# Kernel optimization log

Hardware: AMD Instinct MI355X
Metric: run time of the kernel (lower is better)

The kernel has to match this reference:

```python
import jax, jax.numpy as jnp
import numpy as np
import math

H, DK, DV = 16, 64, 64
D = H * DK  # model_dimension = 1024
N = M = L = 2048


def setup_inputs() -> dict:
    key = jax.random.key(0)
    ks = jax.random.split(key, 12)
    s = 1.0 / math.sqrt(DK)  # keep softmax logits in a sane range
    return {
        "queries": jax.random.normal(ks[0], (N, DK), jnp.float32),
        "keys": jax.random.normal(ks[1], (M, DK), jnp.float32),
        "values": jax.random.normal(ks[2], (L, DV), jnp.float32),
        "Wq": jax.random.normal(ks[3], (H, DK, D), jnp.float32) * s,
        "bq": jax.random.normal(ks[4], (H, D), jnp.float32) * 0.02,
        "Wk": jax.random.normal(ks[5], (H, DK, D), jnp.float32) * s,
        "bk": jax.random.normal(ks[6], (H, D), jnp.float32) * 0.02,
        "Wv": jax.random.normal(ks[7], (H, DV, D), jnp.float32) * s,
        "bv": jax.random.normal(ks[8], (H, D), jnp.float32) * 0.02,
        "Wo": jax.random.normal(ks[9], (D, H * DV), jnp.float32) * (1.0 / math.sqrt(H * DV)),
        "bo": jax.random.normal(ks[10], (D,), jnp.float32) * 0.02,
    }


def reference(queries, keys, values, Wq, bq, Wk, bk, Wv, bv, Wo, bo):
    # Batched per-head projections (original loops over heads in Python).
    Qp = jnp.einsum("nk,hkd->hnd", queries, Wq) + bq[:, None, :]   # (H, N, D)
    Kp = jnp.einsum("mk,hkd->hmd", keys, Wk) + bk[:, None, :]      # (H, M, D)
    Vp = jnp.einsum("lv,hvd->hld", values, Wv) + bv[:, None, :]    # (H, M, D)
    scores = jnp.einsum("hnd,hmd->hnm", Qp, Kp) / math.sqrt(DK)
    attn = jax.nn.softmax(scores, axis=-1)
    heads_out = jnp.einsum("hnm,hmd->hnd", attn, Vp)               # (H, N, D)
    # torch.concat(heads, dim=0).sum(dim=0) == sum over heads AND rows -> (D,)
    pooled = heads_out.sum(axis=(0, 1)).reshape(1, D)
    return pooled @ Wo.T + bo  # (1, D)
```

## Files before the change

kernel.cpp:

```cpp
#include <hip/hip_runtime.h>


typedef __attribute__((ext_vector_type(4))) float floatx4;
typedef __attribute__((ext_vector_type(8))) short shortx8;

__device__ inline unsigned short f2bf(float f) {
    unsigned int u = __float_as_uint(f);
    u += 0x7FFFu + ((u >> 16) & 1u);
    return (unsigned short)(u >> 16);
}
__device__ inline float bf2f(unsigned short s) {
    return __uint_as_float(((unsigned int)s) << 16);
}

__global__ __launch_bounds__(256) void prep_kernel(
    const float* __restrict__ Wq, const float* __restrict__ Wk,
    const float* __restrict__ bq, const float* __restrict__ keys,
    const float* __restrict__ values,
    float* __restrict__ Apart, float* __restrict__ vhpart,
    unsigned short* __restrict__ Kb, unsigned short* __restrict__ VT,
    float* __restrict__ r_ws) {
    const int tid = threadIdx.x;
    const int bx = blockIdx.x;
    __shared__ __align__(16) unsigned char sm[36352];
    if (bx < 128) {
        const int g = bx >> 4, h = bx & 15;
        const int c0 = g * 128;
        unsigned short* wq = (unsigned short*)sm;
        unsigned short* wk = (unsigned short*)(sm + 17408);
        float* bqs = (float*)(sm + 34816);
        float* vred = (float*)(sm + 35328);
        {
            int row = tid >> 2, cs = (tid & 3) * 32;
            const float* wqp = Wq + (size_t)(h * 64 + row) * 1024 + c0 + cs;
            const float* wkp = Wk + (size_t)(h * 64 + row) * 1024 + c0 + cs;
            #pragma unroll
            for (int u = 0; u < 8; ++u) {
                float4 a = *(const float4*)&wqp[u * 4];
                float4 b = *(const float4*)&wkp[u * 4];
                *(ushort4*)&wq[row * 136 + cs + u * 4] =
                    (ushort4){f2bf(a.x), f2bf(a.y), f2bf(a.z), f2bf(a.w)};
                *(ushort4*)&wk[row * 136 + cs + u * 4] =
                    (ushort4){f2bf(b.x), f2bf(b.y), f2bf(b.z), f2bf(b.w)};
            }
            if (tid < 128) bqs[tid] = bq[h * 1024 + c0 + tid];
        }
        __syncthreads();
        const int w = tid >> 6, lane = tid & 63;
        const int ln = lane & 15, quad = lane >> 4;
        {
            const int j = tid & 63, half = tid >> 6;
            float accv = 0.f;
            #pragma unroll
            for (int u = 0; u < 32; ++u)
                accv += bf2f(wk[j * 136 + half * 32 + u]) * bqs[half * 32 + u];
            vred[half * 64 + j] = accv;
        }
        shortx8 af[4];
        #pragma unroll
        for (int kk = 0; kk < 4; ++kk)
            af[kk] = *(shortx8*)&wq[(w * 16 + ln) * 136 + kk * 32 + quad * 8];
        float* ap = Apart + (size_t)bx * 4096;
        #pragma unroll
        for (int cn = 0; cn < 4; ++cn) {
            floatx4 acc = {};
            #pragma unroll
            for (int kk = 0; kk < 4; ++kk) {
                shortx8 bf_ = *(shortx8*)&wk[(cn * 16 + ln) * 136 + kk * 32 + quad * 8];
                acc = __builtin_amdgcn_mfma_f32_16x16x32_bf16(af[kk], bf_, acc, 0, 0, 0);
            }
            #pragma unroll
            for (int r = 0; r < 4; ++r)
                ap[(w * 16 + quad * 4 + r) * 64 + cn * 16 + ln] = acc[r];
        }
        __syncthreads();
        if (tid < 64)
            vhpart[bx * 64 + tid] = vred[tid] + vred[64 + tid] +
                                    vred[128 + tid] + vred[192 + tid];
    } else if (bx < 144) {
        int bk = bx - 128;
        int base = (bk * 256 + tid) * 32;
        #pragma unroll
        for (int u = 0; u < 8; ++u) {
            float4 a = *(const float4*)&keys[base + u * 4];
            *(ushort4*)&Kb[base + u * 4] =
                (ushort4){f2bf(a.x), f2bf(a.y), f2bf(a.z), f2bf(a.w)};
        }
        if (tid < 64) r_ws[bk * 64 + tid] = 0.f;
    } else {
        int bb = bx - 144, m0 = bb * 64;
        unsigned short* vts = (unsigned short*)sm;
        #pragma unroll
        for (int it = 0; it < 4; ++it) {
            int gi = tid + it * 256;
            int m = gi >> 4, c4 = (gi & 15) * 4;
            float4 a = *(const float4*)&values[(size_t)(m0 + m) * 64 + c4];
            vts[(c4 + 0) * 72 + m] = f2bf(a.x);
            vts[(c4 + 1) * 72 + m] = f2bf(a.y);
            vts[(c4 + 2) * 72 + m] = f2bf(a.z);
            vts[(c4 + 3) * 72 + m] = f2bf(a.w);
        }
        __syncthreads();
        #pragma unroll
        for (int it = 0; it < 2; ++it) {
            int gi = tid + it * 256;
            int v = gi >> 3, seg = (gi & 7) * 8;
            *(shortx8*)&VT[v * 2048 + m0 + seg] = *(shortx8*)&vts[v * 72 + seg];
        }
    }
}

__global__ __launch_bounds__(256) void reduceA_kernel(
    const float* __restrict__ Apart, const float* __restrict__ vhpart,
    unsigned short* __restrict__ Atlg, float* __restrict__ vhg) {
    const int tid = threadIdx.x;
    const int h = blockIdx.x >> 2, uq = blockIdx.x & 3;
    #pragma unroll
    for (int uu = 0; uu < 4; ++uu) {
        int e = (uq * 4 + uu) * 256 + tid;
        float s = 0.f;
        #pragma unroll
        for (int g = 0; g < 8; ++g)
            s += Apart[g * 65536 + h * 4096 + e];
        Atlg[h * 4096 + (e & 63) * 64 + (e >> 6)] = f2bf(s);
    }
    if (uq == 0 && tid < 64) {
        float s = 0.f;
        #pragma unroll
        for (int g = 0; g < 8; ++g) s += vhpart[(g * 16 + h) * 64 + tid];
        vhg[h * 64 + tid] = s;
    }
}

#define QSCALE 0.18033688f
__global__ __launch_bounds__(512, 2) void flash_kernel(
    const float* __restrict__ queries, const unsigned short* __restrict__ Atlg,
    const float* __restrict__ vhg, const unsigned short* __restrict__ Kb,
    const unsigned short* __restrict__ VT, float* __restrict__ r_ws) {
    const int h = blockIdx.y;
    const int n0 = blockIdx.x * 128;
    const int tid = threadIdx.x;
    const int w = tid >> 6, lane = tid & 63;
    const int ln = lane & 15, quad = lane >> 4;

    __shared__ __align__(16) unsigned char lds[73728];
    __shared__ float vhs[64];
    unsigned short* Kbuf = (unsigned short*)lds;
    unsigned short* Vbuf = (unsigned short*)(lds + 18432);
    unsigned short* qh   = (unsigned short*)(lds + 36864);
    unsigned short* Pw   = (unsigned short*)(lds + 55296 + w * 2304);
    unsigned short* qstage = (unsigned short*)lds;
    unsigned short* Atl  = (unsigned short*)(lds + 18432);
    float* Rred = (float*)lds;

    {
        int row = tid >> 2, c16 = (tid & 3) * 16;
        const float* qp = queries + (size_t)(n0 + row) * 64 + c16;
        #pragma unroll
        for (int u = 0; u < 4; ++u) {
            float4 a = *(const float4*)&qp[u * 4];
            *(ushort4*)&qstage[row * 72 + c16 + u * 4] =
                (ushort4){f2bf(a.x), f2bf(a.y), f2bf(a.z), f2bf(a.w)};
        }
    }
    {
        int row = tid >> 3, off = (tid & 7) * 8;
        *(shortx8*)&Atl[row * 72 + off] =
            *(const shortx8*)&Atlg[h * 4096 + row * 64 + off];
    }
    if (tid < 64) vhs[tid] = vhg[h * 64 + tid];
    __syncthreads();

    {
        shortx8 qa[2];
        #pragma unroll
        for (int kk = 0; kk < 2; ++kk)
            qa[kk] = *(shortx8*)&qstage[(w * 16 + ln) * 72 + kk * 32 + quad * 8];
        #pragma unroll
        for (int cn = 0; cn < 4; ++cn) {
            floatx4 acc = {};
            #pragma unroll
            for (int kk = 0; kk < 2; ++kk) {
                shortx8 bfr = *(shortx8*)&Atl[(cn * 16 + ln) * 72 + kk * 32 + quad * 8];
                acc = __builtin_amdgcn_mfma_f32_16x16x32_bf16(qa[kk], bfr, acc, 0, 0, 0);
            }
            #pragma unroll
            for (int r = 0; r < 4; ++r)
                qh[(w * 16 + quad * 4 + r) * 72 + cn * 16 + ln] =
                    f2bf((acc[r] + vhs[cn * 16 + ln]) * QSCALE);
        }
    }
    __syncthreads();

    const int srow = tid >> 3, scol = (tid & 7) * 8;
    {
        shortx8 kr = *(const shortx8*)&Kb[(size_t)srow * 64 + scol];
        shortx8 vr = *(const shortx8*)&VT[srow * 2048 + scol];
        *(shortx8*)&Kbuf[srow * 72 + scol] = kr;
        *(shortx8*)&Vbuf[srow * 72 + scol] = vr;
    }
    shortx8 qf[2];
    #pragma unroll
    for (int kk = 0; kk < 2; ++kk)
        qf[kk] = *(shortx8*)&qh[(w * 16 + ln) * 72 + kk * 32 + quad * 8];
    __syncthreads();

    floatx4 O[4] = {};
    float lacc[4] = {};
    for (int s = 0; s < 32; ++s) {
        const int b = s & 1;
        const unsigned short* kb = Kbuf + b * 4608;
        const unsigned short* vb = Vbuf + b * 4608;
        shortx8 krn, vrn;
        if (s < 31) {
            int m0n = (s + 1) * 64;
            krn = *(const shortx8*)&Kb[(size_t)(m0n + srow) * 64 + scol];
            vrn = *(const shortx8*)&VT[srow * 2048 + m0n + scol];
        }
        floatx4 S[4];
        #pragma unroll
        for (int cm = 0; cm < 4; ++cm) {
            floatx4 acc = {};
            #pragma unroll
            for (int kk = 0; kk < 2; ++kk) {
                shortx8 kf = *(const shortx8*)&kb[(cm * 16 + ln) * 72 + kk * 32 + quad * 8];
                acc = __builtin_amdgcn_mfma_f32_16x16x32_bf16(qf[kk], kf, acc, 0, 0, 0);
            }
            S[cm] = acc;
        }
        #pragma unroll
        for (int cm = 0; cm < 4; ++cm) {
            #pragma unroll
            for (int r = 0; r < 4; ++r) {
                float p = __builtin_amdgcn_exp2f(S[cm][r]);
                lacc[r] += p;
                Pw[(quad * 4 + r) * 72 + cm * 16 + ln] = f2bf(p);
            }
        }
        shortx8 pf[2];
        #pragma unroll
        for (int kk = 0; kk < 2; ++kk)
            pf[kk] = *(shortx8*)&Pw[ln * 72 + kk * 32 + quad * 8];
        #pragma unroll
        for (int cv = 0; cv < 4; ++cv) {
            shortx8 v0 = *(const shortx8*)&vb[(cv * 16 + ln) * 72 + quad * 8];
            shortx8 v1 = *(const shortx8*)&vb[(cv * 16 + ln) * 72 + 32 + quad * 8];
            O[cv] = __builtin_amdgcn_mfma_f32_16x16x32_bf16(pf[0], v0, O[cv], 0, 0, 0);
            O[cv] = __builtin_amdgcn_mfma_f32_16x16x32_bf16(pf[1], v1, O[cv], 0, 0, 0);
        }
        if (s < 31) {
            unsigned short* kbn = Kbuf + (b ^ 1) * 4608;
            unsigned short* vbn = Vbuf + (b ^ 1) * 4608;
            *(shortx8*)&kbn[srow * 72 + scol] = krn;
            *(shortx8*)&vbn[srow * 72 + scol] = vrn;
        }
        __syncthreads();
    }

    float linv[4];
    #pragma unroll
    for (int r = 0; r < 4; ++r) {
        float x = lacc[r];
        #pragma unroll
        for (int o = 1; o <= 8; o <<= 1) x += __shfl_xor(x, o);
        linv[r] = 1.0f / x;
    }
    float sacc[4];
    #pragma unroll
    for (int cv = 0; cv < 4; ++cv) {
        float s = 0.f;
        #pragma unroll
        for (int r = 0; r < 4; ++r) s += O[cv][r] * linv[r];
        s += __shfl_xor(s, 16);
        s += __shfl_xor(s, 32);
        sacc[cv] = s;
    }
    __syncthreads();
    if (quad == 0) {
        #pragma unroll
        for (int cv = 0; cv < 4; ++cv)
            Rred[w * 64 + cv * 16 + ln] = sacc[cv];
    }
    __syncthreads();
    if (tid < 64) {
        float s = 0.f;
        #pragma unroll
        for (int g = 0; g < 8; ++g) s += Rred[g * 64 + tid];
        atomicAdd(&r_ws[h * 64 + tid], s);
    }
}

__global__ __launch_bounds__(256) void pool_kernel(
    const float* __restrict__ Wv, const float* __restrict__ bv,
    const float* __restrict__ r_ws, float* __restrict__ pooled) {
    const int tid = threadIdx.x;
    const int d0 = blockIdx.x * 16;
    const int d = tid & 15, hh = tid >> 4;
    __shared__ float red[16][17];
    float acc = bv[hh * 1024 + d0 + d] * 2048.0f;
    const float* rv = r_ws + hh * 64;
    const float* wp = Wv + (size_t)hh * 64 * 1024 + d0 + d;
    #pragma unroll 8
    for (int v = 0; v < 64; ++v) acc += rv[v] * wp[(size_t)v * 1024];
    red[hh][d] = acc;
    __syncthreads();
    if (tid < 16) {
        float s = 0.f;
        #pragma unroll
        for (int g = 0; g < 16; ++g) s += red[g][tid];
        pooled[d0 + tid] = s;
    }
}

__global__ __launch_bounds__(256) void out_kernel(
    const float* __restrict__ Wo, const float* __restrict__ bo,
    const float* __restrict__ pooled, float* __restrict__ out) {
    const int tid = threadIdx.x, w = tid >> 6, lane = tid & 63;
    const int dp = blockIdx.x * 4 + w;
    const float* wr = Wo + (size_t)dp * 1024 + lane * 16;
    const float* pp = pooled + lane * 16;
    float acc = 0.f;
    #pragma unroll
    for (int u = 0; u < 4; ++u) {
        float4 a = *(const float4*)&wr[u * 4];
        float4 p = *(const float4*)&pp[u * 4];
        acc += a.x * p.x + a.y * p.y + a.z * p.z + a.w * p.w;
    }
    #pragma unroll
    for (int o = 32; o > 0; o >>= 1) acc += __shfl_xor(acc, o);
    if (lane == 0) out[dp] = acc + bo[dp];
}

extern "C" void kernel_launch(void* const* d_in, const int* in_sizes, int n_in,
                              void* d_out, int out_size, void* d_ws, size_t ws_size,
                              hipStream_t stream) {
    const float* queries = (const float*)d_in[0];
    const float* keys    = (const float*)d_in[1];
    const float* values  = (const float*)d_in[2];
    const float* Wq      = (const float*)d_in[3];
    const float* bq      = (const float*)d_in[4];
    const float* Wk      = (const float*)d_in[5];
    const float* Wv      = (const float*)d_in[7];
    const float* bv      = (const float*)d_in[8];
    const float* Wo      = (const float*)d_in[9];
    const float* bo      = (const float*)d_in[10];
    float* out = (float*)d_out;

    float* Apart  = (float*)d_ws;
    float* vhpart = Apart + 524288;
    float* r_ws   = vhpart + 8192;
    float* pooled = r_ws + 1024;
    unsigned short* Kb = (unsigned short*)(pooled + 1024);
    unsigned short* VT = Kb + 131072;
    unsigned short* Atlg = VT + 131072;
    float* vhg = (float*)(Atlg + 65536);

    prep_kernel<<<176, 256, 0, stream>>>(Wq, Wk, bq, keys, values,
                                         Apart, vhpart, Kb, VT, r_ws);
    reduceA_kernel<<<64, 256, 0, stream>>>(Apart, vhpart, Atlg, vhg);
    flash_kernel<<<dim3(16, 16), 512, 0, stream>>>(queries, Atlg, vhg,
                                                   Kb, VT, r_ws);
    pool_kernel<<<64, 256, 0, stream>>>(Wv, bv, r_ws, pooled);
    out_kernel<<<256, 256, 0, stream>>>(Wo, bo, pooled, out);
}
```

Before: 132.6 us.

## Process two query tiles per wave and swizzle K/V shared-memory layout

The flash kernel drops from 8 to 4 waves per block, and each wave now computes two 16-row query tiles. Each K and V fragment read from shared memory then feeds two MFMAs, halving LDS reads per unit of math. K/V tiles are stored without padding and with an XOR swizzle to avoid bank conflicts, and the P buffer stride changes. The trade-off is more registers per thread and fewer waves resident to hide latency, with the per-step barrier now covering 4 waves.

```diff
diff --git a/kernel.cpp b/kernel.cpp
--- a/kernel.cpp
+++ b/kernel.cpp
@@ -12,6 +12,8 @@
 __device__ inline float bf2f(unsigned short s) {
     return __uint_as_float(((unsigned int)s) << 16);
 }
+
+#define SWZ(row, bc) ((row) * 128 + ((bc) ^ (((row) & 7) << 4)))
 
 __global__ __launch_bounds__(256) void prep_kernel(
     const float* __restrict__ Wq, const float* __restrict__ Wk,
@@ -133,7 +135,7 @@
 }
 
 #define QSCALE 0.18033688f
-__global__ __launch_bounds__(512, 2) void flash_kernel(
+__global__ __launch_bounds__(256, 1) void flash_kernel(
     const float* __restrict__ queries, const unsigned short* __restrict__ Atlg,
     const float* __restrict__ vhg, const unsigned short* __restrict__ Kb,
     const unsigned short* __restrict__ VT, float* __restrict__ r_ws) {
@@ -143,18 +145,18 @@
     const int w = tid >> 6, lane = tid & 63;
     const int ln = lane & 15, quad = lane >> 4;
 
-    __shared__ __align__(16) unsigned char lds[73728];
+    __shared__ __align__(16) unsigned char lds[70656];
     __shared__ float vhs[64];
-    unsigned short* Kbuf = (unsigned short*)lds;
-    unsigned short* Vbuf = (unsigned short*)(lds + 18432);
-    unsigned short* qh   = (unsigned short*)(lds + 36864);
-    unsigned short* Pw   = (unsigned short*)(lds + 55296 + w * 2304);
+    unsigned short* qh = (unsigned short*)(lds + 32768);
+    unsigned short* Pw = (unsigned short*)(lds + 51200 + w * 4864);
     unsigned short* qstage = (unsigned short*)lds;
-    unsigned short* Atl  = (unsigned short*)(lds + 18432);
+    unsigned short* Atl = (unsigned short*)(lds + 18432);
     float* Rred = (float*)lds;
 
-    {
-        int row = tid >> 2, c16 = (tid & 3) * 16;
+    #pragma unroll
+    for (int it = 0; it < 2; ++it) {
+        int gi = tid + it * 256;
+        int row = gi >> 2, c16 = (gi & 3) * 16;
         const float* qp = queries + (size_t)(n0 + row) * 64 + c16;
         #pragma unroll
         for (int u = 0; u < 4; ++u) {
@@ -163,19 +165,23 @@
                 (ushort4){f2bf(a.x), f2bf(a.y), f2bf(a.z), f2bf(a.w)};
         }
     }
-    {
-        int row = tid >> 3, off = (tid & 7) * 8;
+    #pragma unroll
+    for (int it = 0; it < 2; ++it) {
+        int gi = tid + it * 256;
+        int row = gi >> 3, off = (gi & 7) * 8;
         *(shortx8*)&Atl[row * 72 + off] =
             *(const shortx8*)&Atlg[h * 4096 + row * 64 + off];
     }
     if (tid < 64) vhs[tid] = vhg[h * 64 + tid];
     __syncthreads();
 
-    {
+    #pragma unroll
+    for (int t2 = 0; t2 < 2; ++t2) {
+        const int tt = w * 2 + t2;
         shortx8 qa[2];
         #pragma unroll
         for (int kk = 0; kk < 2; ++kk)
-            qa[kk] = *(shortx8*)&qstage[(w * 16 + ln) * 72 + kk * 32 + quad * 8];
+            qa[kk] = *(shortx8*)&qstage[(tt * 16 + ln) * 72 + kk * 32 + quad * 8];
         #pragma unroll
         for (int cn = 0; cn < 4; ++cn) {
             floatx4 acc = {};
@@ -186,91 +192,114 @@
             }
             #pragma unroll
             for (int r = 0; r < 4; ++r)
-                qh[(w * 16 + quad * 4 + r) * 72 + cn * 16 + ln] =
+                qh[(tt * 16 + quad * 4 + r) * 72 + cn * 16 + ln] =
                     f2bf((acc[r] + vhs[cn * 16 + ln]) * QSCALE);
         }
     }
     __syncthreads();
 
-    const int srow = tid >> 3, scol = (tid & 7) * 8;
+    shortx8 qf[2][2];
+    #pragma unroll
+    for (int t2 = 0; t2 < 2; ++t2)
+        #pragma unroll
+        for (int kk = 0; kk < 2; ++kk)
+            qf[t2][kk] = *(shortx8*)&qh[((w * 2 + t2) * 16 + ln) * 72 + kk * 32 + quad * 8];
+
+    const int srow = tid >> 2;
+    const int sc = (tid & 3) * 16;
     {
-        shortx8 kr = *(const shortx8*)&Kb[(size_t)srow * 64 + scol];
-        shortx8 vr = *(const shortx8*)&VT[srow * 2048 + scol];
-        *(shortx8*)&Kbuf[srow * 72 + scol] = kr;
-        *(shortx8*)&Vbuf[srow * 72 + scol] = vr;
-    }
-    shortx8 qf[2];
-    #pragma unroll
-    for (int kk = 0; kk < 2; ++kk)
-        qf[kk] = *(shortx8*)&qh[(w * 16 + ln) * 72 + kk * 32 + quad * 8];
-    __syncthreads();
-
-    floatx4 O[4] = {};
-    float lacc[4] = {};
+        unsigned char* kb0 = lds;
+        unsigned char* vb0 = lds + 16384;
+        #pragma unroll
+        for (int i = 0; i < 2; ++i) {
+            shortx8 kr = *(const shortx8*)&Kb[(size_t)srow * 64 + sc + i * 8];
+            shortx8 vr = *(const shortx8*)&VT[(size_t)srow * 2048 + sc + i * 8];
+            *(shortx8*)(kb0 + SWZ(srow, sc * 2 + i * 16)) = kr;
+            *(shortx8*)(vb0 + SWZ(srow, sc * 2 + i * 16)) = vr;
+        }
+    }
+    __syncthreads();
+
+    floatx4 O0[4] = {}, O1[4] = {};
+    float lacc0[4] = {}, lacc1[4] = {};
     for (int s = 0; s < 32; ++s) {
         const int b = s & 1;
-        const unsigned short* kb = Kbuf + b * 4608;
-        const unsigned short* vb = Vbuf + b * 4608;
-        shortx8 krn, vrn;
+        const unsigned char* kb = lds + b * 8192;
+        const unsigned char* vb = lds + 16384 + b * 8192;
+        shortx8 krn[2], vrn[2];
         if (s < 31) {
             int m0n = (s + 1) * 64;
-            krn = *(const shortx8*)&Kb[(size_t)(m0n + srow) * 64 + scol];
-            vrn = *(const shortx8*)&VT[srow * 2048 + m0n + scol];
-        }
-        floatx4 S[4];
+            #pragma unroll
+            for (int i = 0; i < 2; ++i) {
+                krn[i] = *(const shortx8*)&Kb[(size_t)(m0n + srow) * 64 + sc + i * 8];
+                vrn[i] = *(const shortx8*)&VT[(size_t)srow * 2048 + m0n + sc + i * 8];
+            }
+        }
+        floatx4 S0[4], S1[4];
         #pragma unroll
         for (int cm = 0; cm < 4; ++cm) {
-            floatx4 acc = {};
-            #pragma unroll
-            for (int kk = 0; kk < 2; ++kk) {
-                shortx8 kf = *(const shortx8*)&kb[(cm * 16 + ln) * 72 + kk * 32 + quad * 8];
-                acc = __builtin_amdgcn_mfma_f32_16x16x32_bf16(qf[kk], kf, acc, 0, 0, 0);
-            }
-            S[cm] = acc;
+            shortx8 kf0 = *(const shortx8*)(kb + SWZ(cm * 16 + ln, quad * 16));
+            shortx8 kf1 = *(const shortx8*)(kb + SWZ(cm * 16 + ln, 64 + quad * 16));
+            floatx4 a0 = {}, a1 = {};
+            a0 = __builtin_amdgcn_mfma_f32_16x16x32_bf16(qf[0][0], kf0, a0, 0, 0, 0);
+            a0 = __builtin_amdgcn_mfma_f32_16x16x32_bf16(qf[0][1], kf1, a0, 0, 0, 0);
+            a1 = __builtin_amdgcn_mfma_f32_16x16x32_bf16(qf[1][0], kf0, a1, 0, 0, 0);
+            a1 = __builtin_amdgcn_mfma_f32_16x16x32_bf16(qf[1][1], kf1, a1, 0, 0, 0);
+            S0[cm] = a0; S1[cm] = a1;
         }
         #pragma unroll
         for (int cm = 0; cm < 4; ++cm) {
             #pragma unroll
             for (int r = 0; r < 4; ++r) {
-                float p = __builtin_amdgcn_exp2f(S[cm][r]);
-                lacc[r] += p;
-                Pw[(quad * 4 + r) * 72 + cm * 16 + ln] = f2bf(p);
-            }
-        }
-        shortx8 pf[2];
-        #pragma unroll
-        for (int kk = 0; kk < 2; ++kk)
-            pf[kk] = *(shortx8*)&Pw[ln * 72 + kk * 32 + quad * 8];
+                float p0 = __builtin_amdgcn_exp2f(S0[cm][r]); lacc0[r] += p0;
+                Pw[(quad * 4 + r) * 76 + cm * 16 + ln] = f2bf(p0);
+                float p1 = __builtin_amdgcn_exp2f(S1[cm][r]); lacc1[r] += p1;
+                Pw[(16 + quad * 4 + r) * 76 + cm * 16 + ln] = f2bf(p1);
+            }
+        }
+        shortx8 pf[2][2];
+        #pragma unroll
+        for (int t2 = 0; t2 < 2; ++t2)
+            #pragma unroll
+            for (int kk = 0; kk < 2; ++kk)
+                pf[t2][kk] = *(shortx8*)&Pw[(t2 * 16 + ln) * 76 + kk * 32 + quad * 8];
         #pragma unroll
         for (int cv = 0; cv < 4; ++cv) {
-            shortx8 v0 = *(const shortx8*)&vb[(cv * 16 + ln) * 72 + quad * 8];
-            shortx8 v1 = *(const shortx8*)&vb[(cv * 16 + ln) * 72 + 32 + quad * 8];
-            O[cv] = __builtin_amdgcn_mfma_f32_16x16x32_bf16(pf[0], v0, O[cv], 0, 0, 0);
-            O[cv] = __builtin_amdgcn_mfma_f32_16x16x32_bf16(pf[1], v1, O[cv], 0, 0, 0);
+            shortx8 v0 = *(const shortx8*)(vb + SWZ(cv * 16 + ln, quad * 16));
+            shortx8 v1 = *(const shortx8*)(vb + SWZ(cv * 16 + ln, 64 + quad * 16));
+            O0[cv] = __builtin_amdgcn_mfma_f32_16x16x32_bf16(pf[0][0], v0, O0[cv], 0, 0, 0);
+            O0[cv] = __builtin_amdgcn_mfma_f32_16x16x32_bf16(pf[0][1], v1, O0[cv], 0, 0, 0);
+            O1[cv] = __builtin_amdgcn_mfma_f32_16x16x32_bf16(pf[1][0], v0, O1[cv], 0, 0, 0);
+            O1[cv] = __builtin_amdgcn_mfma_f32_16x16x32_bf16(pf[1][1], v1, O1[cv], 0, 0, 0);
         }
         if (s < 31) {
-            unsigned short* kbn = Kbuf + (b ^ 1) * 4608;
-            unsigned short* vbn = Vbuf + (b ^ 1) * 4608;
-            *(shortx8*)&kbn[srow * 72 + scol] = krn;
-            *(shortx8*)&vbn[srow * 72 + scol] = vrn;
+            unsigned char* kbn = lds + (b ^ 1) * 8192;
+            unsigned char* vbn = lds + 16384 + (b ^ 1) * 8192;
+            #pragma unroll
+            for (int i = 0; i < 2; ++i) {
+                *(shortx8*)(kbn + SWZ(srow, sc * 2 + i * 16)) = krn[i];
+                *(shortx8*)(vbn + SWZ(srow, sc * 2 + i * 16)) = vrn[i];
+            }
         }
         __syncthreads();
     }
 
-    float linv[4];
+    float linv0[4], linv1[4];
     #pragma unroll
     for (int r = 0; r < 4; ++r) {
-        float x = lacc[r];
-        #pragma unroll
-        for (int o = 1; o <= 8; o <<= 1) x += __shfl_xor(x, o);
-        linv[r] = 1.0f / x;
+        float x0 = lacc0[r], x1 = lacc1[r];
+        #pragma unroll
+        for (int o = 1; o <= 8; o <<= 1) { x0 += __shfl_xor(x0, o); x1 += __shfl_xor(x1, o); }
+        linv0[r] = 1.0f / x0;
+        linv1[r] = 1.0f / x1;
     }
     float sacc[4];
     #pragma unroll
     for (int cv = 0; cv < 4; ++cv) {
         float s = 0.f;
         #pragma unroll
-        for (int r = 0; r < 4; ++r) s += O[cv][r] * linv[r];
+        for (int r = 0; r < 4; ++r)
+            s += O0[cv][r] * linv0[r] + O1[cv][r] * linv1[r];
         s += __shfl_xor(s, 16);
         s += __shfl_xor(s, 32);
         sacc[cv] = s;
@@ -283,9 +312,7 @@
     }
     __syncthreads();
     if (tid < 64) {
-        float s = 0.f;
-        #pragma unroll
-        for (int g = 0; g < 8; ++g) s += Rred[g * 64 + tid];
+        float s = Rred[tid] + Rred[64 + tid] + Rred[128 + tid] + Rred[192 + tid];
         atomicAdd(&r_ws[h * 64 + tid], s);
     }
 }
@@ -358,7 +385,7 @@
     prep_kernel<<<176, 256, 0, stream>>>(Wq, Wk, bq, keys, values,
                                          Apart, vhpart, Kb, VT, r_ws);
     reduceA_kernel<<<64, 256, 0, stream>>>(Apart, vhpart, Atlg, vhg);
-    flash_kernel<<<dim3(16, 16), 512, 0, stream>>>(queries, Atlg, vhg,
+    flash_kernel<<<dim3(16, 16), 256, 0, stream>>>(queries, Atlg, vhg,
                                                    Kb, VT, r_ws);
     pool_kernel<<<64, 256, 0, stream>>>(Wv, bv, r_ws, pooled);
     out_kernel<<<256, 256, 0, stream>>>(Wo, bo, pooled, out);
```

New measurement: 152.5 us. 15.0% more time.

## Split flash attention into row-sum pass and column-weight pass, drop PV matmul

Applied to the files above, without the earlier changes.

Because the output only needs attention summed over query rows, the attention-times-V product is restructured. A first pass computes the softmax denominators per query row. A second pass computes per-key column weights sum_n P[n,m]/l[n] by recomputing the scores, then takes the weighted sum of value rows in fp32. This removes the PV MFMA, the P staging through LDS and the V transpose prep, and LDS is swizzled to avoid bank conflicts. In exchange the QK^T exponentials are computed twice and there is one extra kernel launch plus a Q round-trip through global memory.

```diff
diff --git a/kernel.cpp b/kernel.cpp
--- a/kernel.cpp
+++ b/kernel.cpp
@@ -13,13 +13,14 @@
     return __uint_as_float(((unsigned int)s) << 16);
 }
 
+#define SWZ(row, bc) ((row) * 128 + ((bc) ^ (((row) & 7) << 4)))
+#define QSCALE 0.18033688f
+
 __global__ __launch_bounds__(256) void prep_kernel(
     const float* __restrict__ Wq, const float* __restrict__ Wk,
     const float* __restrict__ bq, const float* __restrict__ keys,
-    const float* __restrict__ values,
     float* __restrict__ Apart, float* __restrict__ vhpart,
-    unsigned short* __restrict__ Kb, unsigned short* __restrict__ VT,
-    float* __restrict__ r_ws) {
+    unsigned short* __restrict__ Kb, float* __restrict__ r_ws) {
     const int tid = threadIdx.x;
     const int bx = blockIdx.x;
     __shared__ __align__(16) unsigned char sm[36352];
@@ -77,7 +78,7 @@
         if (tid < 64)
             vhpart[bx * 64 + tid] = vred[tid] + vred[64 + tid] +
                                     vred[128 + tid] + vred[192 + tid];
-    } else if (bx < 144) {
+    } else {
         int bk = bx - 128;
         int base = (bk * 256 + tid) * 32;
         #pragma unroll
@@ -87,26 +88,6 @@
                 (ushort4){f2bf(a.x), f2bf(a.y), f2bf(a.z), f2bf(a.w)};
         }
         if (tid < 64) r_ws[bk * 64 + tid] = 0.f;
-    } else {
-        int bb = bx - 144, m0 = bb * 64;
-        unsigned short* vts = (unsigned short*)sm;
-        #pragma unroll
-        for (int it = 0; it < 4; ++it) {
-            int gi = tid + it * 256;
-            int m = gi >> 4, c4 = (gi & 15) * 4;
-            float4 a = *(const float4*)&values[(size_t)(m0 + m) * 64 + c4];
-            vts[(c4 + 0) * 72 + m] = f2bf(a.x);
-            vts[(c4 + 1) * 72 + m] = f2bf(a.y);
-            vts[(c4 + 2) * 72 + m] = f2bf(a.z);
-            vts[(c4 + 3) * 72 + m] = f2bf(a.w);
-        }
-        __syncthreads();
-        #pragma unroll
-        for (int it = 0; it < 2; ++it) {
-            int gi = tid + it * 256;
-            int v = gi >> 3, seg = (gi & 7) * 8;
-            *(shortx8*)&VT[v * 2048 + m0 + seg] = *(shortx8*)&vts[v * 72 + seg];
-        }
     }
 }
 
@@ -132,26 +113,21 @@
     }
 }
 
-#define QSCALE 0.18033688f
-__global__ __launch_bounds__(512, 2) void flash_kernel(
+__global__ __launch_bounds__(256, 4) void pass1_kernel(
     const float* __restrict__ queries, const unsigned short* __restrict__ Atlg,
     const float* __restrict__ vhg, const unsigned short* __restrict__ Kb,
-    const unsigned short* __restrict__ VT, float* __restrict__ r_ws) {
+    unsigned short* __restrict__ Qhs, float* __restrict__ u_ws) {
     const int h = blockIdx.y;
-    const int n0 = blockIdx.x * 128;
+    const int n0 = blockIdx.x * 64;
     const int tid = threadIdx.x;
     const int w = tid >> 6, lane = tid & 63;
     const int ln = lane & 15, quad = lane >> 4;
 
-    __shared__ __align__(16) unsigned char lds[73728];
+    __shared__ __align__(16) unsigned char lds[27648];
     __shared__ float vhs[64];
-    unsigned short* Kbuf = (unsigned short*)lds;
-    unsigned short* Vbuf = (unsigned short*)(lds + 18432);
-    unsigned short* qh   = (unsigned short*)(lds + 36864);
-    unsigned short* Pw   = (unsigned short*)(lds + 55296 + w * 2304);
     unsigned short* qstage = (unsigned short*)lds;
-    unsigned short* Atl  = (unsigned short*)(lds + 18432);
-    float* Rred = (float*)lds;
+    unsigned short* Atl = (unsigned short*)(lds + 9216);
+    unsigned short* qh = (unsigned short*)(lds + 18432);
 
     {
         int row = tid >> 2, c16 = (tid & 3) * 16;
@@ -162,11 +138,10 @@
             *(ushort4*)&qstage[row * 72 + c16 + u * 4] =
                 (ushort4){f2bf(a.x), f2bf(a.y), f2bf(a.z), f2bf(a.w)};
         }
-    }
-    {
-        int row = tid >> 3, off = (tid & 7) * 8;
-        *(shortx8*)&Atl[row * 72 + off] =
-            *(const shortx8*)&Atlg[h * 4096 + row * 64 + off];
+        #pragma unroll
+        for (int u = 0; u < 2; ++u)
+            *(shortx8*)&Atl[row * 72 + c16 + u * 8] =
+                *(const shortx8*)&Atlg[h * 4096 + row * 64 + c16 + u * 8];
     }
     if (tid < 64) vhs[tid] = vhg[h * 64 + tid];
     __syncthreads();
@@ -192,102 +167,142 @@
     }
     __syncthreads();
 
-    const int srow = tid >> 3, scol = (tid & 7) * 8;
-    {
-        shortx8 kr = *(const shortx8*)&Kb[(size_t)srow * 64 + scol];
-        shortx8 vr = *(const shortx8*)&VT[srow * 2048 + scol];
-        *(shortx8*)&Kbuf[srow * 72 + scol] = kr;
-        *(shortx8*)&Vbuf[srow * 72 + scol] = vr;
-    }
+    #pragma unroll
+    for (int k = 0; k < 2; ++k) {
+        int seg = tid * 2 + k, row = seg >> 3, off = (seg & 7) * 8;
+        *(shortx8*)&Qhs[((size_t)h * 2048 + n0 + row) * 64 + off] =
+            *(shortx8*)&qh[row * 72 + off];
+    }
+    const int srow = tid >> 2, sc = (tid & 3) * 16;
+    #pragma unroll
+    for (int i = 0; i < 2; ++i)
+        *(shortx8*)(lds + SWZ(srow, sc * 2 + i * 16)) =
+            *(const shortx8*)&Kb[(size_t)srow * 64 + sc + i * 8];
     shortx8 qf[2];
     #pragma unroll
     for (int kk = 0; kk < 2; ++kk)
         qf[kk] = *(shortx8*)&qh[(w * 16 + ln) * 72 + kk * 32 + quad * 8];
     __syncthreads();
 
-    floatx4 O[4] = {};
     float lacc[4] = {};
     for (int s = 0; s < 32; ++s) {
-        const int b = s & 1;
-        const unsigned short* kb = Kbuf + b * 4608;
-        const unsigned short* vb = Vbuf + b * 4608;
-        shortx8 krn, vrn;
+        const unsigned char* kb = lds + (s & 1) * 8192;
+        shortx8 krn[2];
         if (s < 31) {
             int m0n = (s + 1) * 64;
-            krn = *(const shortx8*)&Kb[(size_t)(m0n + srow) * 64 + scol];
-            vrn = *(const shortx8*)&VT[srow * 2048 + m0n + scol];
-        }
-        floatx4 S[4];
+            #pragma unroll
+            for (int i = 0; i < 2; ++i)
+                krn[i] = *(const shortx8*)&Kb[(size_t)(m0n + srow) * 64 + sc + i * 8];
+        }
         #pragma unroll
         for (int cm = 0; cm < 4; ++cm) {
+            shortx8 kf0 = *(const shortx8*)(kb + SWZ(cm * 16 + ln, quad * 16));
+            shortx8 kf1 = *(const shortx8*)(kb + SWZ(cm * 16 + ln, 64 + quad * 16));
             floatx4 acc = {};
-            #pragma unroll
-            for (int kk = 0; kk < 2; ++kk) {
-                shortx8 kf = *(const shortx8*)&kb[(cm * 16 + ln) * 72 + kk * 32 + quad * 8];
-                acc = __builtin_amdgcn_mfma_f32_16x16x32_bf16(qf[kk], kf, acc, 0, 0, 0);
-            }
-            S[cm] = acc;
-        }
-        #pragma unroll
-        for (int cm = 0; cm < 4; ++cm) {
-            #pragma unroll
-            for (int r = 0; r < 4; ++r) {
-                float p = __builtin_amdgcn_exp2f(S[cm][r]);
-                lacc[r] += p;
-                Pw[(quad * 4 + r) * 72 + cm * 16 + ln] = f2bf(p);
-            }
-        }
-        shortx8 pf[2];
-        #pragma unroll
-        for (int kk = 0; kk < 2; ++kk)
-            pf[kk] = *(shortx8*)&Pw[ln * 72 + kk * 32 + quad * 8];
-        #pragma unroll
-        for (int cv = 0; cv < 4; ++cv) {
-            shortx8 v0 = *(const shortx8*)&vb[(cv * 16 + ln) * 72 + quad * 8];
-            shortx8 v1 = *(const shortx8*)&vb[(cv * 16 + ln) * 72 + 32 + quad * 8];
-            O[cv] = __builtin_amdgcn_mfma_f32_16x16x32_bf16(pf[0], v0, O[cv], 0, 0, 0);
-            O[cv] = __builtin_amdgcn_mfma_f32_16x16x32_bf16(pf[1], v1, O[cv], 0, 0, 0);
+            acc = __builtin_amdgcn_mfma_f32_16x16x32_bf16(qf[0], kf0, acc, 0, 0, 0);
+            acc = __builtin_amdgcn_mfma_f32_16x16x32_bf16(qf[1], kf1, acc, 0, 0, 0);
+            #pragma unroll
+            for (int r = 0; r < 4; ++r)
+                lacc[r] += __builtin_amdgcn_exp2f(acc[r]);
         }
         if (s < 31) {
-            unsigned short* kbn = Kbuf + (b ^ 1) * 4608;
-            unsigned short* vbn = Vbuf + (b ^ 1) * 4608;
-            *(shortx8*)&kbn[srow * 72 + scol] = krn;
-            *(shortx8*)&vbn[srow * 72 + scol] = vrn;
+            unsigned char* kbn = lds + (((s & 1) ^ 1)) * 8192;
+            #pragma unroll
+            for (int i = 0; i < 2; ++i)
+                *(shortx8*)(kbn + SWZ(srow, sc * 2 + i * 16)) = krn[i];
         }
         __syncthreads();
     }
 
-    float linv[4];
     #pragma unroll
     for (int r = 0; r < 4; ++r) {
         float x = lacc[r];
         #pragma unroll
         for (int o = 1; o <= 8; o <<= 1) x += __shfl_xor(x, o);
-        linv[r] = 1.0f / x;
-    }
-    float sacc[4];
-    #pragma unroll
-    for (int cv = 0; cv < 4; ++cv) {
-        float s = 0.f;
-        #pragma unroll
-        for (int r = 0; r < 4; ++r) s += O[cv][r] * linv[r];
-        s += __shfl_xor(s, 16);
-        s += __shfl_xor(s, 32);
-        sacc[cv] = s;
-    }
-    __syncthreads();
-    if (quad == 0) {
-        #pragma unroll
-        for (int cv = 0; cv < 4; ++cv)
-            Rred[w * 64 + cv * 16 + ln] = sacc[cv];
-    }
-    __syncthreads();
-    if (tid < 64) {
-        float s = 0.f;
-        #pragma unroll
-        for (int g = 0; g < 8; ++g) s += Rred[g * 64 + tid];
-        atomicAdd(&r_ws[h * 64 + tid], s);
-    }
+        if (ln == 0)
+            u_ws[(size_t)h * 2048 + n0 + w * 16 + quad * 4 + r] = 1.0f / x;
+    }
+}
+
+__global__ __launch_bounds__(256, 4) void pass2_kernel(
+    const unsigned short* __restrict__ Qhs, const float* __restrict__ u_ws,
+    const unsigned short* __restrict__ Kb, const float* __restrict__ values,
+    float* __restrict__ r_ws) {
+    const int h = blockIdx.y;
+    const int mb = blockIdx.x * 64;
+    const int tid = threadIdx.x;
+    const int w = tid >> 6, lane = tid & 63;
+    const int ln = lane & 15, quad = lane >> 4;
+
+    __shared__ __align__(16) unsigned char lds[18176];
+    float* u_sb = (float*)(lds + 16384);
+    float* g_s = (float*)(lds + 16896);
+    float* Rred = (float*)(lds + 17152);
+
+    shortx8 kf[2];
+    #pragma unroll
+    for (int kk = 0; kk < 2; ++kk)
+        kf[kk] = *(const shortx8*)&Kb[(size_t)(mb + w * 16 + ln) * 64 + kk * 32 + quad * 8];
+
+    const int srow = tid >> 2, sc = (tid & 3) * 16;
+    #pragma unroll
+    for (int i = 0; i < 2; ++i)
+        *(shortx8*)(lds + SWZ(srow, sc * 2 + i * 16)) =
+            *(const shortx8*)&Qhs[((size_t)h * 2048 + srow) * 64 + sc + i * 8];
+    if (tid < 64) u_sb[tid] = u_ws[(size_t)h * 2048 + tid];
+    __syncthreads();
+
+    float gacc = 0.f;
+    for (int s = 0; s < 32; ++s) {
+        const unsigned char* qb = lds + (s & 1) * 8192;
+        const float* us = u_sb + (s & 1) * 64;
+        shortx8 qrn[2];
+        float urn = 0.f;
+        if (s < 31) {
+            int n0n = (s + 1) * 64;
+            #pragma unroll
+            for (int i = 0; i < 2; ++i)
+                qrn[i] = *(const shortx8*)&Qhs[((size_t)h * 2048 + n0n + srow) * 64 + sc + i * 8];
+            if (tid < 64) urn = u_ws[(size_t)h * 2048 + n0n + tid];
+        }
+        #pragma unroll
+        for (int rt = 0; rt < 4; ++rt) {
+            shortx8 qa0 = *(const shortx8*)(qb + SWZ(rt * 16 + ln, quad * 16));
+            shortx8 qa1 = *(const shortx8*)(qb + SWZ(rt * 16 + ln, 64 + quad * 16));
+            floatx4 acc = {};
+            acc = __builtin_amdgcn_mfma_f32_16x16x32_bf16(qa0, kf[0], acc, 0, 0, 0);
+            acc = __builtin_amdgcn_mfma_f32_16x16x32_bf16(qa1, kf[1], acc, 0, 0, 0);
+            #pragma unroll
+            for (int r = 0; r < 4; ++r)
+                gacc += __builtin_amdgcn_exp2f(acc[r]) * us[rt * 16 + quad * 4 + r];
+        }
+        if (s < 31) {
+            unsigned char* qbn = lds + (((s & 1) ^ 1)) * 8192;
+            #pragma unroll
+            for (int i = 0; i < 2; ++i)
+                *(shortx8*)(qbn + SWZ(srow, sc * 2 + i * 16)) = qrn[i];
+            if (tid < 64) u_sb[((s & 1) ^ 1) * 64 + tid] = urn;
+        }
+        __syncthreads();
+    }
+
+    gacc += __shfl_xor(gacc, 16);
+    gacc += __shfl_xor(gacc, 32);
+    if (quad == 0) g_s[w * 16 + ln] = gacc;
+    __syncthreads();
+    {
+        int grp = tid >> 6, v = tid & 63;
+        float acc = 0.f;
+        #pragma unroll
+        for (int j = 0; j < 16; ++j)
+            acc += g_s[grp * 16 + j] *
+                   values[(size_t)(mb + grp * 16 + j) * 64 + v];
+        Rred[grp * 64 + v] = acc;
+    }
+    __syncthreads();
+    if (tid < 64)
+        atomicAdd(&r_ws[h * 64 + tid],
+                  Rred[tid] + Rred[64 + tid] + Rred[128 + tid] + Rred[192 + tid]);
 }
 
 __global__ __launch_bounds__(256) void pool_kernel(
@@ -346,20 +361,23 @@
     const float* bo      = (const float*)d_in[10];
     float* out = (float*)d_out;
 
-    float* Apart  = (float*)d_ws;
+    char* base = (char*)d_ws;
+    unsigned short* Qhs = (unsigned short*)base;
+    float* Apart  = (float*)base;
     float* vhpart = Apart + 524288;
-    float* r_ws   = vhpart + 8192;
-    float* pooled = r_ws + 1024;
-    unsigned short* Kb = (unsigned short*)(pooled + 1024);
-    unsigned short* VT = Kb + 131072;
-    unsigned short* Atlg = VT + 131072;
-    float* vhg = (float*)(Atlg + 65536);
-
-    prep_kernel<<<176, 256, 0, stream>>>(Wq, Wk, bq, keys, values,
-                                         Apart, vhpart, Kb, VT, r_ws);
+    float* u_ws   = (float*)(base + 4194304);
+    float* r_ws   = (float*)(base + 4325376);
+    float* pooled = (float*)(base + 4329472);
+    unsigned short* Kb   = (unsigned short*)(base + 4333568);
+    unsigned short* Atlg = (unsigned short*)(base + 4595712);
+    float* vhg    = (float*)(base + 4726784);
+
+    prep_kernel<<<144, 256, 0, stream>>>(Wq, Wk, bq, keys,
+                                         Apart, vhpart, Kb, r_ws);
     reduceA_kernel<<<64, 256, 0, stream>>>(Apart, vhpart, Atlg, vhg);
-    flash_kernel<<<dim3(16, 16), 512, 0, stream>>>(queries, Atlg, vhg,
-                                                   Kb, VT, r_ws);
+    pass1_kernel<<<dim3(32, 16), 256, 0, stream>>>(queries, Atlg, vhg,
+                                                   Kb, Qhs, u_ws);
+    pass2_kernel<<<dim3(32, 16), 256, 0, stream>>>(Qhs, u_ws, Kb, values, r_ws);
     pool_kernel<<<64, 256, 0, stream>>>(Wv, bv, r_ws, pooled);
     out_kernel<<<256, 256, 0, stream>>>(Wo, bo, pooled, out);
 }
```

New measurement: 137.7 us. 1.04x slower.
